# Performance work log

Measured on AMD Instinct MI355X. Metric: run time of the kernel, lower is better.

## Reference

```python
import jax, jax.numpy as jnp
import numpy as np


def _ln(x, g, b, eps=1e-5):
    mu = jnp.mean(x, axis=-1, keepdims=True)
    var = jnp.mean((x - mu) ** 2, axis=-1, keepdims=True)
    return (x - mu) * jax.lax.rsqrt(var + eps) * g + b


def setup_inputs() -> dict:
    key = jax.random.key(0)
    ks = jax.random.split(key, 12)
    B, H, W, D = 16, 128, 128, 64
    N = H * W
    Dff = 4 * D
    s = 0.02
    f32 = jnp.float32
    return {
        "x": jax.random.normal(ks[0], (B, N, D), f32),
        "H": H,
        "W": W,
        "ln1_scale": jnp.ones((D,), f32),
        "ln1_bias": jnp.zeros((D,), f32),
        "Wk": jax.random.normal(ks[1], (D, D), f32) * s,
        "bk": jnp.zeros((D,), f32),
        "Wq": jax.random.normal(ks[2], (D, D), f32) * s,
        "bq": jnp.zeros((D,), f32),
        "Wv": jax.random.normal(ks[3], (D, D), f32) * s,
        "bv": jnp.zeros((D,), f32),
        "Wr": jax.random.normal(ks[4], (D, D), f32) * s,
        "br": jnp.zeros((D,), f32),
        "ln2_scale": jnp.ones((D,), f32),
        "ln2_bias": jnp.zeros((D,), f32),
        "W1": jax.random.normal(ks[5], (Dff, D), f32) * s,
        "b1": jnp.zeros((Dff,), f32),
        "dw_w": jax.random.normal(ks[6], (Dff, 1, 3, 3), f32) * s,
        "dw_b": jnp.zeros((Dff,), f32),
        "W2": jax.random.normal(ks[7], (D, Dff), f32) * s,
        "b2": jnp.zeros((D,), f32),
    }


def reference(x, H, W, ln1_scale, ln1_bias, Wk, bk, Wq, bq, Wv, bv, Wr, br,
              ln2_scale, ln2_bias, W1, b1, dw_w, dw_b, W2, b2):
    B, N, D = x.shape
    Dff = W1.shape[0]

    # ---- EfficientAttention (head_count=1), tokens kept as [B, N, C] ----
    n1 = _ln(x, ln1_scale, ln1_bias)
    # 1x1 convs on [B,D,H,W] == per-token linear projections
    k = jax.nn.softmax(n1 @ Wk.T + bk, axis=1)    # softmax over spatial dim N (torch dim=2 of [B,Ck,N])
    q = jax.nn.softmax(n1 @ Wq.T + bq, axis=-1)   # softmax over key channels (torch dim=1)
    v = n1 @ Wv.T + bv                            # [B,N,Cv]
    context = jnp.einsum('bnk,bnv->bkv', k, v)    # key @ value^T, tiny [B,Ck,Cv]
    att = jnp.einsum('bkv,bnk->bnv', context, q)  # context^T @ query -> [B,N,Cv]
    attn_out = att @ Wr.T + br                    # reprojection 1x1 conv
    tx = x + attn_out

    # ---- MixFFN: fc1 -> depthwise 3x3 -> GELU -> fc2 ----
    n2 = _ln(tx, ln2_scale, ln2_bias)
    h = n2 @ W1.T + b1                            # [B,N,Dff]
    himg = jnp.transpose(h, (0, 2, 1)).reshape(B, Dff, H, W)
    conv = jax.lax.conv_general_dilated(
        himg, dw_w, window_strides=(1, 1), padding='SAME',
        feature_group_count=Dff,
        dimension_numbers=('NCHW', 'OIHW', 'NCHW')) + dw_b[None, :, None, None]
    h2 = jnp.transpose(conv.reshape(B, Dff, N), (0, 2, 1))
    h2 = jax.nn.gelu(h2, approximate=False)       # torch nn.GELU default is exact erf
    out = tx + (h2 @ W2.T + b2)
    return out
```

## Files before the change

kernel.cpp:

```cpp
#include <hip/hip_runtime.h>
#include <math.h>

typedef __bf16 bf16x8 __attribute__((ext_vector_type(8)));
typedef float f32x4 __attribute__((ext_vector_type(4)));
typedef float f32x2 __attribute__((ext_vector_type(2)));
typedef unsigned short u16x8 __attribute__((ext_vector_type(8)));
typedef unsigned short u16x4v __attribute__((ext_vector_type(4)));

constexpr int NIMG = 16384;
constexpr int HPITCH = 130;

__device__ __forceinline__ unsigned short f2bf(float f){
  unsigned u = __builtin_bit_cast(unsigned, f);
  u += 0x7fffu + ((u>>16)&1u);
  return (unsigned short)(u>>16);
}
__device__ __forceinline__ unsigned pack2(float a, float b){
  return (unsigned)f2bf(a) | ((unsigned)f2bf(b)<<16);
}
__device__ __forceinline__ float bf2f(unsigned short h){
  unsigned u = ((unsigned)h)<<16;
  return __builtin_bit_cast(float, u);
}
__device__ __forceinline__ bf16x8 ldfrag_g(const unsigned short* p){
  u16x8 v = *reinterpret_cast<const u16x8*>(p);
  return __builtin_bit_cast(bf16x8, v);
}
__device__ __forceinline__ f32x4 mfma16(bf16x8 a, bf16x8 b, f32x4 c){
  return __builtin_amdgcn_mfma_f32_16x16x32_bf16(a, b, c, 0, 0, 0);
}


__global__ __launch_bounds__(64) void k0_wfrag(
  const float* __restrict__ Wk, const float* __restrict__ Wq,
  const float* __restrict__ Wv, const float* __restrict__ Wr,
  const float* __restrict__ W1, const float* __restrict__ W2,
  const float* __restrict__ dww, const float* __restrict__ dwb,
  float* __restrict__ dwp, unsigned short* __restrict__ wf)
{
  const int bid = blockIdx.x, l = threadIdx.x;
  if (bid == 96){
    #pragma unroll
    for (int h=0; h<2; ++h){
      int cp = l + h*64;
      #pragma unroll
      for (int b=0; b<2; ++b){
        int slot = 2*cp + b;
        int f = ((slot&15)<<4) | (slot>>4);
        #pragma unroll
        for (int j=0;j<9;++j) dwp[cp*24 + j*2 + b] = dww[f*9+j];
        dwp[cp*24 + 18 + b] = dwb[f];
        dwp[cp*24 + 20 + b] = 0.f;
        dwp[cp*24 + 22 + b] = 0.f;
      }
    }
    return;
  }
  const float* src; int K, nt, ks; unsigned short* dst; bool perm = false;
  if (bid < 32){
    int w = bid>>3, f = bid&7;
    src = (w==0)?Wk:(w==1)?Wq:(w==2)?Wv:Wr;
    K = 64; nt = f>>1; ks = f&1;
    dst = wf + w*4096 + f*512;
  } else if (bid < 64){
    int f = bid-32; src = W1; K = 64; nt = f>>1; ks = f&1;
    dst = wf + 16384 + f*512;
  } else {
    int f = bid-64; src = W2; K = 256; nt = f>>3; ks = f&7;
    dst = wf + 32768 + f*512; perm = true;
  }
  u16x8 v;
  #pragma unroll
  for (int j=0;j<8;++j){
    int k = ks*32 + (l>>4)*8 + j;
    if (perm) k = ((k&15)<<4) | (k>>4);
    int n = nt*16 + (l&15);
    v[j] = f2bf(src[n*K + k]);
  }
  *reinterpret_cast<u16x8*>(dst + l*8) = v;
}

__global__ __launch_bounds__(256) void zhalo(unsigned* __restrict__ gh, unsigned* __restrict__ zr){
  int idx = blockIdx.x*256 + threadIdx.x;
  if (idx < 262144){
    int ch = idx & 63;
    int pos = idx >> 6;
    int side = pos & 1, row = pos >> 1;
    gh[(size_t)(row*HPITCH + side*(HPITCH-1))*64 + ch] = 0;
  } else {
    int j = idx - 262144;
    if (j < 8320) zr[j] = 0;
  }
}

__global__ __launch_bounds__(256,2) void k1_ctx(
  const float* __restrict__ x, const float* __restrict__ g1, const float* __restrict__ be1,
  const float* __restrict__ bk, const float* __restrict__ bv,
  const unsigned short* __restrict__ wf,
  float* __restrict__ g_part, float* __restrict__ g_sump)
{
  __shared__ unsigned short tiles[4][4096];
  float* ctx_l  = reinterpret_cast<float*>(&tiles[0][0]);
  float* ssum_l = ctx_l + 64*68;
  const int t = threadIdx.x, wid = t>>6, l = t&63;
  const int lg = l>>4, l15 = l&15;
  unsigned short* tile = tiles[wid];
  const int tok0 = blockIdx.x*256 + wid*64;

  bf16x8 WkF[8], WvF[8];
  #pragma unroll
  for (int f=0; f<8; ++f){
    WkF[f] = ldfrag_g(wf +    0 + f*512 + l*8);
    WvF[f] = ldfrag_g(wf + 8192 + f*512 + l*8);
  }
  float4 g1v  = *reinterpret_cast<const float4*>(&g1[l15*4]);
  float4 be1v = *reinterpret_cast<const float4*>(&be1[l15*4]);
  float bkv[4], bvv[4];
  #pragma unroll
  for (int ct=0; ct<4; ++ct){ bkv[ct]=bk[ct*16+l15]; bvv[ct]=bv[ct*16+l15]; }

  f32x4 acc[4][4];
  #pragma unroll
  for (int a=0;a<4;++a)
    #pragma unroll
    for (int b=0;b<4;++b) acc[a][b] = (f32x4){0.f,0.f,0.f,0.f};
  float sume[4] = {0.f,0.f,0.f,0.f};

  #pragma unroll
  for (int it=0; it<16; ++it){
    int row = it*4 + lg;
    float4 xv = *reinterpret_cast<const float4*>(&x[(size_t)(tok0+row)*64 + l15*4]);
    float s1 = xv.x+xv.y+xv.z+xv.w;
    float s2 = xv.x*xv.x + xv.y*xv.y + xv.z*xv.z + xv.w*xv.w;
    #pragma unroll
    for (int off=1; off<16; off<<=1){ s1 += __shfl_xor(s1,off,64); s2 += __shfl_xor(s2,off,64); }
    float mu = s1*(1.f/64.f);
    float rs = rsqrtf(s2*(1.f/64.f) - mu*mu + 1e-5f);
    uint2 pk = { pack2((xv.x-mu)*rs*g1v.x + be1v.x, (xv.y-mu)*rs*g1v.y + be1v.y),
                 pack2((xv.z-mu)*rs*g1v.z + be1v.z, (xv.w-mu)*rs*g1v.w + be1v.w) };
    *reinterpret_cast<uint2*>(&tile[row*64 + ((l15*4) ^ ((row&7)<<3))]) = pk;
  }
  bf16x8 aF[4][2];
  #pragma unroll
  for (int mt=0;mt<4;++mt){
    int row = mt*16+l15, sw=(row&7)<<3, ab=row*64;
    aF[mt][0] = __builtin_bit_cast(bf16x8, *reinterpret_cast<const u16x8*>(tile+ab+((     lg*8)^sw)));
    aF[mt][1] = __builtin_bit_cast(bf16x8, *reinterpret_cast<const u16x8*>(tile+ab+((32 + lg*8)^sw)));
  }
  #pragma unroll
  for (int half=0; half<2; ++half){
    #pragma unroll
    for (int m2=0;m2<2;++m2){
      const int mt = half*2+m2;
      #pragma unroll
      for (int ct=0;ct<4;++ct){
        f32x4 z = {0.f,0.f,0.f,0.f};
        z = mfma16(aF[mt][0], WkF[ct*2+0], z);
        z = mfma16(aF[mt][1], WkF[ct*2+1], z);
        float e0=__expf(z[0]+bkv[ct]), e1=__expf(z[1]+bkv[ct]);
        float e2=__expf(z[2]+bkv[ct]), e3=__expf(z[3]+bkv[ct]);
        sume[ct] += (e0+e1)+(e2+e3);
        const int c = ct*16+l15, sw = (c&7)<<3;
        const int cb = m2*16+lg*4;
        uint2 pe = { pack2(e0,e1), pack2(e2,e3) };
        *reinterpret_cast<uint2*>(&tile[c*64 + (cb ^ sw)]) = pe;
        f32x4 w = {0.f,0.f,0.f,0.f};
        w = mfma16(aF[mt][0], WvF[ct*2+0], w);
        w = mfma16(aF[mt][1], WvF[ct*2+1], w);
        uint2 pv = { pack2(w[0]+bvv[ct], w[1]+bvv[ct]), pack2(w[2]+bvv[ct], w[3]+bvv[ct]) };
        *reinterpret_cast<uint2*>(&tile[c*64 + ((32+cb) ^ sw)]) = pv;
      }
    }
    bf16x8 eA[4], vB[4];
    #pragma unroll
    for (int cm=0;cm<4;++cm){
      int row = cm*16+l15, sw=(row&7)<<3;
      eA[cm] = __builtin_bit_cast(bf16x8, *reinterpret_cast<const u16x8*>(tile + row*64 + ((     lg*8)^sw)));
      vB[cm] = __builtin_bit_cast(bf16x8, *reinterpret_cast<const u16x8*>(tile + row*64 + ((32 + lg*8)^sw)));
    }
    #pragma unroll
    for (int cm=0; cm<4; ++cm)
      #pragma unroll
      for (int jn=0; jn<4; ++jn)
        acc[cm][jn] = mfma16(eA[cm], vB[jn], acc[cm][jn]);
  }

  __syncthreads();
  #pragma unroll
  for (int ct=0; ct<4; ++ct){
    float s = sume[ct];
    s += __shfl_xor(s,16,64); s += __shfl_xor(s,32,64);
    if (lg==0) ssum_l[wid*64 + ct*16+l15] = s;
  }
  #define CTX_RED(OP) \
    _Pragma("unroll") for (int cm=0;cm<4;++cm) \
    _Pragma("unroll") for (int jn=0;jn<4;++jn) \
    _Pragma("unroll") for (int r=0;r<4;++r) \
      ctx_l[(cm*16+lg*4+r)*68 + jn*16+l15] OP acc[cm][jn][r];
  if (wid==0){ CTX_RED(=) }  __syncthreads();
  if (wid==1){ CTX_RED(+=) } __syncthreads();
  if (wid==2){ CTX_RED(+=) } __syncthreads();
  if (wid==3){ CTX_RED(+=) } __syncthreads();
  #undef CTX_RED
  for (int i=t; i<4096; i+=256)
    g_part[(size_t)blockIdx.x*4096 + i] = ctx_l[(i>>6)*68 + (i&63)];
  if (t<64)
    g_sump[blockIdx.x*64 + t] = ssum_l[t] + ssum_l[64+t] + ssum_l[128+t] + ssum_l[192+t];
}

__global__ __launch_bounds__(512) void k15_ctxwr(
  const float* __restrict__ g_part, const float* __restrict__ g_sump,
  const float* __restrict__ Wr, unsigned short* __restrict__ ctxWrF)
{
  __shared__ float sctx[4096];
  __shared__ float sWr[4096];
  __shared__ float sinv[64];
  const int b = blockIdx.x, t = threadIdx.x;
  if (t<64){
    float s=0.f;
    #pragma unroll 8
    for (int p=0;p<64;++p) s += g_sump[(b*64+p)*64 + t];
    sinv[t] = 1.f/s;
  }
  for (int idx=t; idx<4096; idx+=512){
    float s=0.f;
    #pragma unroll 8
    for (int p=0;p<64;++p) s += g_part[(size_t)(b*64+p)*4096 + idx];
    sctx[idx] = s;
  }
  __syncthreads();
  {
    int c = t>>3, d0 = (t&7)*8;
    float invc = sinv[c];
    #pragma unroll
    for (int dd=0; dd<8; ++dd){
      int d = d0+dd; float s = 0.f;
      #pragma unroll
      for (int v=0; v<64; ++v) s += sctx[c*64+v]*Wr[d*64+v];
      sWr[c*64+d] = s*invc;
    }
  }
  __syncthreads();
  {
    int f = t>>6, l = t&63, nt = f>>1, ks = f&1;
    u16x8 v;
    #pragma unroll
    for (int j=0;j<8;++j){
      int k = ks*32 + (l>>4)*8 + j;
      int n = nt*16 + (l&15);
      v[j] = f2bf(sWr[k*64+n]);
    }
    *reinterpret_cast<u16x8*>(ctxWrF + b*4096 + f*512 + l*8) = v;
  }
}

__global__ __launch_bounds__(256,2) void k2_attn_ffn1(
  const float* __restrict__ x,
  const float* __restrict__ g1, const float* __restrict__ be1,
  const float* __restrict__ bq, const float* __restrict__ br,
  const float* __restrict__ g2, const float* __restrict__ be2,
  const float* __restrict__ b1,
  const unsigned short* __restrict__ wf,
  const unsigned short* __restrict__ ctxWrF,
  unsigned short* __restrict__ g_txb, unsigned char* __restrict__ g_h)
{
  __shared__ unsigned short tiles[4][4096];
  const int t = threadIdx.x, wid = t>>6, l = t&63;
  const int l15 = l&15, lg = l>>4;
  unsigned short* tile = tiles[wid];
  const int tok0 = (blockIdx.x*4 + wid)*64;
  const int img  = blockIdx.x>>6;
  const int yrow = (tok0>>7)&127;
  const int xb   = tok0&127;
  const size_t hbase = ((size_t)(img*128 + yrow)*HPITCH + 1 + xb)*256;

  bf16x8 WqF[8], CWF[8];
  #pragma unroll
  for (int f=0; f<8; ++f){
    WqF[f] = ldfrag_g(wf + 4096 + f*512 + l*8);
    CWF[f] = ldfrag_g(ctxWrF + img*4096 + f*512 + l*8);
  }
  float4 g1v  = *reinterpret_cast<const float4*>(&g1[l15*4]);
  float4 be1v = *reinterpret_cast<const float4*>(&be1[l15*4]);
  float bqv[4], brv[4], g2v[4], be2v[4];
  #pragma unroll
  for (int nt=0; nt<4; ++nt){
    bqv[nt]=bq[nt*16+l15]; brv[nt]=br[nt*16+l15];
    g2v[nt]=g2[nt*16+l15]; be2v[nt]=be2[nt*16+l15];
  }
  float b1v[16];
  #pragma unroll
  for (int i=0;i<16;++i) b1v[i]=b1[i*16+l15];

  #pragma unroll
  for (int it=0; it<16; ++it){
    int row = it*4 + lg;
    float4 xv = *reinterpret_cast<const float4*>(&x[(size_t)(tok0+row)*64 + l15*4]);
    float s1 = xv.x+xv.y+xv.z+xv.w;
    float s2 = xv.x*xv.x + xv.y*xv.y + xv.z*xv.z + xv.w*xv.w;
    #pragma unroll
    for (int off=1; off<16; off<<=1){ s1 += __shfl_xor(s1,off,64); s2 += __shfl_xor(s2,off,64); }
    float mu = s1*(1.f/64.f);
    float rs = rsqrtf(s2*(1.f/64.f) - mu*mu + 1e-5f);
    uint2 pk = { pack2((xv.x-mu)*rs*g1v.x + be1v.x, (xv.y-mu)*rs*g1v.y + be1v.y),
                 pack2((xv.z-mu)*rs*g1v.z + be1v.z, (xv.w-mu)*rs*g1v.w + be1v.w) };
    *reinterpret_cast<uint2*>(&tile[row*64 + ((l15*4) ^ ((row&7)<<3))]) = pk;
  }

  for (int mt=0; mt<4; ++mt){
    const int arow = mt*16 + l15;
    const int asw  = (arow&7)<<3;
    const int abase= arow*64;
    bf16x8 a0 = __builtin_bit_cast(bf16x8, *reinterpret_cast<const u16x8*>(tile + abase + ((     lg*8) ^ asw)));
    bf16x8 a1 = __builtin_bit_cast(bf16x8, *reinterpret_cast<const u16x8*>(tile + abase + ((32 + lg*8) ^ asw)));
    f32x4 qa[4];
    #pragma unroll
    for (int nt=0; nt<4; ++nt){
      f32x4 z = {0.f,0.f,0.f,0.f};
      z = mfma16(a0, WqF[nt*2+0], z);
      z = mfma16(a1, WqF[nt*2+1], z);
      qa[nt] = z;
    }
    #pragma unroll
    for (int nt=0; nt<4; ++nt)
      #pragma unroll
      for (int r=0; r<4; ++r) qa[nt][r] += bqv[nt];
    float mx[4];
    #pragma unroll
    for (int r=0;r<4;++r) mx[r] = fmaxf(fmaxf(qa[0][r],qa[1][r]), fmaxf(qa[2][r],qa[3][r]));
    #pragma unroll
    for (int off=1; off<16; off<<=1)
      #pragma unroll
      for (int r=0;r<4;++r) mx[r] = fmaxf(mx[r], __shfl_xor(mx[r], off, 64));
    float sm[4] = {0.f,0.f,0.f,0.f};
    #pragma unroll
    for (int nt=0;nt<4;++nt)
      #pragma unroll
      for (int r=0;r<4;++r){ float e = __expf(qa[nt][r]-mx[r]); qa[nt][r]=e; sm[r]+=e; }
    #pragma unroll
    for (int off=1; off<16; off<<=1)
      #pragma unroll
      for (int r=0;r<4;++r) sm[r] += __shfl_xor(sm[r], off, 64);
    float inv[4];
    #pragma unroll
    for (int r=0;r<4;++r) inv[r] = 1.f/sm[r];
    #pragma unroll
    for (int nt=0;nt<4;++nt)
      #pragma unroll
      for (int r=0;r<4;++r){
        int row = mt*16 + lg*4 + r, col = nt*16 + l15;
        tile[row*64 + (col ^ ((row&7)<<3))] = f2bf(qa[nt][r]*inv[r]);
      }
    bf16x8 p0 = __builtin_bit_cast(bf16x8, *reinterpret_cast<const u16x8*>(tile + abase + ((     lg*8) ^ asw)));
    bf16x8 p1 = __builtin_bit_cast(bf16x8, *reinterpret_cast<const u16x8*>(tile + abase + ((32 + lg*8) ^ asw)));
    f32x4 ao[4];
    #pragma unroll
    for (int nt=0; nt<4; ++nt){
      f32x4 z = {0.f,0.f,0.f,0.f};
      z = mfma16(p0, CWF[nt*2+0], z);
      z = mfma16(p1, CWF[nt*2+1], z);
      ao[nt] = z;
    }
    float txv[4][4];
    float s1v[4] = {0.f,0.f,0.f,0.f}, s2v[4] = {0.f,0.f,0.f,0.f};
    #pragma unroll
    for (int nt=0;nt<4;++nt)
      #pragma unroll
      for (int r=0;r<4;++r){
        size_t row = (size_t)(tok0 + mt*16 + lg*4 + r);
        float v = ao[nt][r] + brv[nt] + x[row*64 + nt*16+l15];
        g_txb[row*64 + nt*16+l15] = f2bf(v);
        txv[nt][r] = v; s1v[r] += v; s2v[r] += v*v;
      }
    #pragma unroll
    for (int off=1; off<16; off<<=1)
      #pragma unroll
      for (int r=0;r<4;++r){ s1v[r] += __shfl_xor(s1v[r], off, 64); s2v[r] += __shfl_xor(s2v[r], off, 64); }
    #pragma unroll
    for (int r=0;r<4;++r){
      float mu2 = s1v[r]*(1.f/64.f);
      float rs  = rsqrtf(s2v[r]*(1.f/64.f) - mu2*mu2 + 1e-5f);
      s1v[r] = mu2; s2v[r] = rs;
    }
    #pragma unroll
    for (int nt=0;nt<4;++nt)
      #pragma unroll
      for (int r=0;r<4;++r){
        int row = mt*16 + lg*4 + r, col = nt*16 + l15;
        float n2 = (txv[nt][r]-s1v[r])*s2v[r]*g2v[nt] + be2v[nt];
        tile[row*64 + (col ^ ((row&7)<<3))] = f2bf(n2);
      }
  }

  for (int mt=0; mt<4; ++mt){
    const int arow = mt*16 + l15;
    const int asw  = (arow&7)<<3;
    const int abase= arow*64;
    bf16x8 n20 = __builtin_bit_cast(bf16x8, *reinterpret_cast<const u16x8*>(tile + abase + ((     lg*8) ^ asw)));
    bf16x8 n21 = __builtin_bit_cast(bf16x8, *reinterpret_cast<const u16x8*>(tile + abase + ((32 + lg*8) ^ asw)));
    unsigned hq[4][4];
    #pragma unroll
    for (int np=0; np<8; ++np){
      bf16x8 wa0 = ldfrag_g(wf + 16384 + (np*4+0)*512 + l*8);
      bf16x8 wa1 = ldfrag_g(wf + 16384 + (np*4+1)*512 + l*8);
      bf16x8 wb0 = ldfrag_g(wf + 16384 + (np*4+2)*512 + l*8);
      bf16x8 wb1 = ldfrag_g(wf + 16384 + (np*4+3)*512 + l*8);
      float ba = b1v[np*2], bb = b1v[np*2+1];
      f32x4 ha = {ba,ba,ba,ba};
      ha = mfma16(n20, wa0, ha);
      ha = mfma16(n21, wa1, ha);
      f32x4 hb = {bb,bb,bb,bb};
      hb = mfma16(n20, wb0, hb);
      hb = mfma16(n21, wb1, hb);
      const int d = np>>1;
      if ((np&1)==0){
        #pragma unroll
        for (int r=0;r<4;++r)
          hq[r][d] = (unsigned)__builtin_amdgcn_cvt_pk_fp8_f32(ha[r], hb[r], 0, false);
      } else {
        #pragma unroll
        for (int r=0;r<4;++r)
          hq[r][d] = (unsigned)__builtin_amdgcn_cvt_pk_fp8_f32(ha[r], hb[r], (int)hq[r][d], true);
      }
    }
    #pragma unroll
    for (int r=0;r<4;++r){
      const size_t ro = hbase + (size_t)(mt*16+lg*4+r)*256 + l15*16;
      uint4 v = { hq[r][0], hq[r][1], hq[r][2], hq[r][3] };
      *reinterpret_cast<uint4*>(g_h + ro) = v;
    }
  }
}

__global__ __launch_bounds__(256,4) void k3_conv_ffn2(
  const unsigned char* __restrict__ g_h,
  const unsigned char* __restrict__ zrow,
  const float* __restrict__ dwp,
  const float* __restrict__ b2,
  const unsigned short* __restrict__ wf,
  const unsigned short* __restrict__ g_txb, float* __restrict__ out)
{
  __shared__ unsigned ring[4][1170];
  __shared__ unsigned short obuf[2][4096];
  const int t = threadIdx.x, w = t>>6, l = t&63;
  const int l15 = l&15, lg = l>>4;
  const int bid = (blockIdx.x & 7)*128 + (blockIdx.x >> 3);
  const int img = bid>>6;
  const int r6  = bid&63;
  const int y0  = (r6>>3)*16, x0 = (r6&7)*16;

  const int cp = t & 127;
  const int pg = t >> 7;
  f32x2 tp[9];
  #pragma unroll
  for (int j=0;j<9;++j)
    tp[j] = *reinterpret_cast<const f32x2*>(&dwp[cp*24 + j*2]);
  const f32x2 cb2 = *reinterpret_cast<const f32x2*>(&dwp[cp*24 + 18]);

  bf16x8 W2F[8];
  #pragma unroll
  for (int q=0;q<8;++q)
    W2F[q] = ldfrag_g(wf + 32768 + (w*8 + q)*512 + l*8);
  const float4 b2q = *reinterpret_cast<const float4*>(&b2[w*16 + lg*4]);

  const int pi = 1 + (t>>4);
  const int c0 = (t&15)*16;

  auto rowsrc = [&](int ri) -> const unsigned char* {
    return (ri>=0 && ri<128)
      ? g_h + ((size_t)(img*128+ri)*HPITCH + x0)*256
      : zrow + x0*256;
  };
  auto ldrow = [&](int ri, uint4* m, unsigned* h){
    const unsigned char* src = rowsrc(ri);
    *m = *reinterpret_cast<const uint4*>(src + pi*256 + c0);
    if (t < 128){
      int ph = (t<64)?0:17, dh = t&63;
      *h = reinterpret_cast<const unsigned*>(src + ph*256)[dh];
    }
  };
  auto wrrow = [&](int sl, uint4 m, unsigned h){
    unsigned* rg = ring[sl];
    const int base = pi*65 + (c0>>2);
    rg[base+0] = m.x; rg[base+1] = m.y; rg[base+2] = m.z; rg[base+3] = m.w;
    if (t < 128){
      int ph = (t<64)?0:17, dh = t&63;
      rg[ph*65 + dh] = h;
    }
  };

  {
    uint4 m0,m1,m2; unsigned h0=0,h1=0,h2=0;
    ldrow(y0-1,&m0,&h0); ldrow(y0,&m1,&h1); ldrow(y0+1,&m2,&h2);
    wrrow(0,m0,h0); wrrow(1,m1,h1); wrrow(2,m2,h2);
  }
  __syncthreads();

  const f32x2 kC0 = {-2.3022082f,-2.3022082f};
  const f32x2 kC1 = {-0.1029432f,-0.1029432f};

  for (int yy=0; yy<16; ++yy){
    const int gy = y0 + yy;
    uint4 rm; unsigned rh = 0;
    ldrow(gy+2, &rm, &rh);
    const size_t gtok = (size_t)img*16384 + (size_t)gy*128 + x0 + l15;
    const u16x4v tq = *reinterpret_cast<const u16x4v*>(&g_txb[gtok*64 + w*16 + lg*4]);

    {
      const unsigned short* rA = reinterpret_cast<const unsigned short*>(ring[(yy  )&3]);
      const unsigned short* rB = reinterpret_cast<const unsigned short*>(ring[(yy+1)&3]);
      const unsigned short* rC = reinterpret_cast<const unsigned short*>(ring[(yy+2)&3]);
      unsigned short* ob = obuf[yy&1];
      const int rb = pg*8;
      f32x2 PA = __builtin_amdgcn_cvt_pk_f32_fp8((int)rA[(rb  )*130 + cp], false);
      f32x2 PB = __builtin_amdgcn_cvt_pk_f32_fp8((int)rB[(rb  )*130 + cp], false);
      f32x2 PC = __builtin_amdgcn_cvt_pk_f32_fp8((int)rC[(rb  )*130 + cp], false);
      f32x2 CA = __builtin_amdgcn_cvt_pk_f32_fp8((int)rA[(rb+1)*130 + cp], false);
      f32x2 CB = __builtin_amdgcn_cvt_pk_f32_fp8((int)rB[(rb+1)*130 + cp], false);
      f32x2 CC = __builtin_amdgcn_cvt_pk_f32_fp8((int)rC[(rb+1)*130 + cp], false);
      #pragma unroll
      for (int i=0;i<8;++i){
        const int ro = (rb+i+2)*130 + cp;
        f32x2 NA = __builtin_amdgcn_cvt_pk_f32_fp8((int)rA[ro], false);
        f32x2 NB = __builtin_amdgcn_cvt_pk_f32_fp8((int)rB[ro], false);
        f32x2 NC = __builtin_amdgcn_cvt_pk_f32_fp8((int)rC[ro], false);
        f32x2 a = cb2;
        a += tp[0]*PA; a += tp[1]*CA; a += tp[2]*NA;
        a += tp[3]*PB; a += tp[4]*CB; a += tp[5]*NB;
        a += tp[6]*PC; a += tp[7]*CC; a += tp[8]*NC;
        f32x2 u = a*a;
        f32x2 wv = u*kC1 + kC0;
        f32x2 arg = a*wv;
        f32x2 e;
        e[0]=__builtin_amdgcn_exp2f(arg[0]); e[1]=__builtin_amdgcn_exp2f(arg[1]);
        f32x2 den = e + (f32x2){1.f,1.f};
        f32x2 rc;
        rc[0]=__builtin_amdgcn_rcpf(den[0]); rc[1]=__builtin_amdgcn_rcpf(den[1]);
        f32x2 g = a*rc;
        unsigned pk;
        asm("v_cvt_pk_bf16_f32 %0, %1, %2" : "=v"(pk) : "v"(g[0]), "v"(g[1]));
        const int p = rb + i;
        *reinterpret_cast<unsigned*>(&ob[p*256 + ((2*cp) ^ ((p&7)<<3))]) = pk;
        PA=CA; PB=CB; PC=CC; CA=NA; CB=NB; CC=NC;
      }
    }

    wrrow((yy+3)&3, rm, rh);
    __syncthreads();

    f32x4 oacc = {0.f,0.f,0.f,0.f};
    const int nsw = (l15&7)<<3;
    const unsigned short* ob = obuf[yy&1];
    #pragma unroll
    for (int i=0;i<4;++i){
      bf16x8 fb0 = __builtin_bit_cast(bf16x8,
        *reinterpret_cast<const u16x8*>(&ob[l15*256 + ((i*64      + lg*8) ^ nsw)]));
      bf16x8 fb1 = __builtin_bit_cast(bf16x8,
        *reinterpret_cast<const u16x8*>(&ob[l15*256 + ((i*64 + 32 + lg*8) ^ nsw)]));
      oacc = mfma16(W2F[i*2+0], fb0, oacc);
      oacc = mfma16(W2F[i*2+1], fb1, oacc);
    }
    float4 o;
    o.x = oacc[0] + b2q.x + bf2f(tq[0]);
    o.y = oacc[1] + b2q.y + bf2f(tq[1]);
    o.z = oacc[2] + b2q.z + bf2f(tq[2]);
    o.w = oacc[3] + b2q.w + bf2f(tq[3]);
    *reinterpret_cast<float4*>(&out[gtok*64 + w*16 + lg*4]) = o;
  }
}

extern "C" void kernel_launch(void* const* d_in, const int* in_sizes, int n_in,
                              void* d_out, int out_size, void* d_ws, size_t ws_size,
                              hipStream_t stream)
{
  const float* x  =(const float*)d_in[0];
  const float* g1 =(const float*)d_in[3];
  const float* be1=(const float*)d_in[4];
  const float* Wk =(const float*)d_in[5];
  const float* bk =(const float*)d_in[6];
  const float* Wq =(const float*)d_in[7];
  const float* bq =(const float*)d_in[8];
  const float* Wv =(const float*)d_in[9];
  const float* bv =(const float*)d_in[10];
  const float* Wr =(const float*)d_in[11];
  const float* br =(const float*)d_in[12];
  const float* g2 =(const float*)d_in[13];
  const float* be2=(const float*)d_in[14];
  const float* W1 =(const float*)d_in[15];
  const float* b1 =(const float*)d_in[16];
  const float* dww=(const float*)d_in[17];
  const float* dwb=(const float*)d_in[18];
  const float* W2 =(const float*)d_in[19];
  const float* b2 =(const float*)d_in[20];
  float* outp = (float*)d_out;
  char* ws = (char*)d_ws;

  unsigned short* wfb    = (unsigned short*)ws;
  unsigned short* ctxWrF = (unsigned short*)(ws + 98304);
  float* g_sump = (float*)(ws + 229376);
  float* g_part = (float*)(ws + 524288);
  unsigned short* g_txb = (unsigned short*)(ws + 17825792);
  unsigned char* g_h    = (unsigned char*)(ws + 51380224);
  unsigned char* zr     = (unsigned char*)(ws + 119537664);
  float* dwp            = (float*)(ws + 119603200);

  hipLaunchKernelGGL(k0_wfrag, dim3(97), dim3(64), 0, stream, Wk, Wq, Wv, Wr, W1, W2, dww, dwb, dwp, wfb);
  hipLaunchKernelGGL(zhalo, dim3(1057), dim3(256), 0, stream, (unsigned*)g_h, (unsigned*)zr);
  hipLaunchKernelGGL(k1_ctx, dim3(1024), dim3(256), 0, stream, x, g1, be1, bk, bv, wfb, g_part, g_sump);
  hipLaunchKernelGGL(k15_ctxwr, dim3(16), dim3(512), 0, stream, g_part, g_sump, Wr, ctxWrF);
  hipLaunchKernelGGL(k2_attn_ffn1, dim3(1024), dim3(256), 0, stream,
                     x, g1, be1, bq, br, g2, be2, b1, wfb, ctxWrF, g_txb, g_h);
  hipLaunchKernelGGL(k3_conv_ffn2, dim3(1024), dim3(256), 0, stream,
                     g_h, zr, dwp, b2, wfb, g_txb, outp);
}
```

Measured before the change: 203.3 us.

## Compute query softmax in k1 and pass it to k2 through global memory

Moves the query projection and its softmax from k2 into k1, which already holds the LayerNorm-1 tile. The result is written to a new bf16 global buffer, so k2 no longer recomputes LN1 or Q; it loads the softmaxed query fragments directly. This removes the duplicated LayerNorm and Q matmul work from k2. In exchange it adds a 32 MB write in k1 and a matching read in k2, and k1 gains extra work and register pressure.

New measurement: 203.5 us. Within noise of the previous version (+0.1%).

```diff
diff --git a/kernel.cpp b/kernel.cpp
--- a/kernel.cpp
+++ b/kernel.cpp
@@ -95,9 +95,10 @@
 
 __global__ __launch_bounds__(256,2) void k1_ctx(
   const float* __restrict__ x, const float* __restrict__ g1, const float* __restrict__ be1,
-  const float* __restrict__ bk, const float* __restrict__ bv,
+  const float* __restrict__ bk, const float* __restrict__ bq, const float* __restrict__ bv,
   const unsigned short* __restrict__ wf,
-  float* __restrict__ g_part, float* __restrict__ g_sump)
+  float* __restrict__ g_part, float* __restrict__ g_sump,
+  unsigned short* __restrict__ qs)
 {
   __shared__ unsigned short tiles[4][4096];
   float* ctx_l  = reinterpret_cast<float*>(&tiles[0][0]);
@@ -107,24 +108,8 @@
   unsigned short* tile = tiles[wid];
   const int tok0 = blockIdx.x*256 + wid*64;
 
-  bf16x8 WkF[8], WvF[8];
-  #pragma unroll
-  for (int f=0; f<8; ++f){
-    WkF[f] = ldfrag_g(wf +    0 + f*512 + l*8);
-    WvF[f] = ldfrag_g(wf + 8192 + f*512 + l*8);
-  }
   float4 g1v  = *reinterpret_cast<const float4*>(&g1[l15*4]);
   float4 be1v = *reinterpret_cast<const float4*>(&be1[l15*4]);
-  float bkv[4], bvv[4];
-  #pragma unroll
-  for (int ct=0; ct<4; ++ct){ bkv[ct]=bk[ct*16+l15]; bvv[ct]=bv[ct*16+l15]; }
-
-  f32x4 acc[4][4];
-  #pragma unroll
-  for (int a=0;a<4;++a)
-    #pragma unroll
-    for (int b=0;b<4;++b) acc[a][b] = (f32x4){0.f,0.f,0.f,0.f};
-  float sume[4] = {0.f,0.f,0.f,0.f};
 
   #pragma unroll
   for (int it=0; it<16; ++it){
@@ -147,6 +132,78 @@
     aF[mt][0] = __builtin_bit_cast(bf16x8, *reinterpret_cast<const u16x8*>(tile+ab+((     lg*8)^sw)));
     aF[mt][1] = __builtin_bit_cast(bf16x8, *reinterpret_cast<const u16x8*>(tile+ab+((32 + lg*8)^sw)));
   }
+
+  {
+    float bqv[4];
+    #pragma unroll
+    for (int ct=0; ct<4; ++ct) bqv[ct]=bq[ct*16+l15];
+    #pragma unroll
+    for (int mt=0; mt<4; ++mt){
+      f32x4 qa[4];
+      #pragma unroll
+      for (int nt=0; nt<4; ++nt){
+        bf16x8 w0 = ldfrag_g(wf + 4096 + (nt*2+0)*512 + l*8);
+        bf16x8 w1 = ldfrag_g(wf + 4096 + (nt*2+1)*512 + l*8);
+        f32x4 z = {0.f,0.f,0.f,0.f};
+        z = mfma16(aF[mt][0], w0, z);
+        z = mfma16(aF[mt][1], w1, z);
+        #pragma unroll
+        for (int r=0;r<4;++r) z[r] += bqv[nt];
+        qa[nt] = z;
+      }
+      float mx[4];
+      #pragma unroll
+      for (int r=0;r<4;++r) mx[r] = fmaxf(fmaxf(qa[0][r],qa[1][r]), fmaxf(qa[2][r],qa[3][r]));
+      #pragma unroll
+      for (int off=1; off<16; off<<=1)
+        #pragma unroll
+        for (int r=0;r<4;++r) mx[r] = fmaxf(mx[r], __shfl_xor(mx[r], off, 64));
+      float sm[4] = {0.f,0.f,0.f,0.f};
+      #pragma unroll
+      for (int nt=0;nt<4;++nt)
+        #pragma unroll
+        for (int r=0;r<4;++r){ float e = __expf(qa[nt][r]-mx[r]); qa[nt][r]=e; sm[r]+=e; }
+      #pragma unroll
+      for (int off=1; off<16; off<<=1)
+        #pragma unroll
+        for (int r=0;r<4;++r) sm[r] += __shfl_xor(sm[r], off, 64);
+      float inv[4];
+      #pragma unroll
+      for (int r=0;r<4;++r) inv[r] = 1.f/sm[r];
+      #pragma unroll
+      for (int nt=0;nt<4;++nt)
+        #pragma unroll
+        for (int r=0;r<4;++r){
+          int row = mt*16 + lg*4 + r, col = nt*16 + l15;
+          tile[row*64 + (col ^ ((row&7)<<3))] = f2bf(qa[nt][r]*inv[r]);
+        }
+    }
+    #pragma unroll
+    for (int c=0;c<8;++c){
+      int idx = c*64 + l;
+      int tok = idx>>3, b8 = (idx&7)*8;
+      u16x8 v = *reinterpret_cast<const u16x8*>(tile + tok*64 + (b8 ^ ((tok&7)<<3)));
+      *reinterpret_cast<u16x8*>(qs + (size_t)(tok0+tok)*64 + b8) = v;
+    }
+  }
+
+  bf16x8 WkF[8], WvF[8];
+  #pragma unroll
+  for (int f=0; f<8; ++f){
+    WkF[f] = ldfrag_g(wf +    0 + f*512 + l*8);
+    WvF[f] = ldfrag_g(wf + 8192 + f*512 + l*8);
+  }
+  float bkv[4], bvv[4];
+  #pragma unroll
+  for (int ct=0; ct<4; ++ct){ bkv[ct]=bk[ct*16+l15]; bvv[ct]=bv[ct*16+l15]; }
+
+  f32x4 acc[4][4];
+  #pragma unroll
+  for (int a=0;a<4;++a)
+    #pragma unroll
+    for (int b=0;b<4;++b) acc[a][b] = (f32x4){0.f,0.f,0.f,0.f};
+  float sume[4] = {0.f,0.f,0.f,0.f};
+
   #pragma unroll
   for (int half=0; half<2; ++half){
     #pragma unroll
@@ -256,12 +313,12 @@
 
 __global__ __launch_bounds__(256,2) void k2_attn_ffn1(
   const float* __restrict__ x,
-  const float* __restrict__ g1, const float* __restrict__ be1,
-  const float* __restrict__ bq, const float* __restrict__ br,
+  const float* __restrict__ br,
   const float* __restrict__ g2, const float* __restrict__ be2,
   const float* __restrict__ b1,
   const unsigned short* __restrict__ wf,
   const unsigned short* __restrict__ ctxWrF,
+  const unsigned short* __restrict__ qs,
   unsigned short* __restrict__ g_txb, unsigned char* __restrict__ g_h)
 {
   __shared__ unsigned short tiles[4][4096];
@@ -274,85 +331,24 @@
   const int xb   = tok0&127;
   const size_t hbase = ((size_t)(img*128 + yrow)*HPITCH + 1 + xb)*256;
 
-  bf16x8 WqF[8], CWF[8];
-  #pragma unroll
-  for (int f=0; f<8; ++f){
-    WqF[f] = ldfrag_g(wf + 4096 + f*512 + l*8);
+  bf16x8 CWF[8];
+  #pragma unroll
+  for (int f=0; f<8; ++f)
     CWF[f] = ldfrag_g(ctxWrF + img*4096 + f*512 + l*8);
-  }
-  float4 g1v  = *reinterpret_cast<const float4*>(&g1[l15*4]);
-  float4 be1v = *reinterpret_cast<const float4*>(&be1[l15*4]);
-  float bqv[4], brv[4], g2v[4], be2v[4];
+  float brv[4], g2v[4], be2v[4];
   #pragma unroll
   for (int nt=0; nt<4; ++nt){
-    bqv[nt]=bq[nt*16+l15]; brv[nt]=br[nt*16+l15];
+    brv[nt]=br[nt*16+l15];
     g2v[nt]=g2[nt*16+l15]; be2v[nt]=be2[nt*16+l15];
   }
   float b1v[16];
   #pragma unroll
   for (int i=0;i<16;++i) b1v[i]=b1[i*16+l15];
 
-  #pragma unroll
-  for (int it=0; it<16; ++it){
-    int row = it*4 + lg;
-    float4 xv = *reinterpret_cast<const float4*>(&x[(size_t)(tok0+row)*64 + l15*4]);
-    float s1 = xv.x+xv.y+xv.z+xv.w;
-    float s2 = xv.x*xv.x + xv.y*xv.y + xv.z*xv.z + xv.w*xv.w;
-    #pragma unroll
-    for (int off=1; off<16; off<<=1){ s1 += __shfl_xor(s1,off,64); s2 += __shfl_xor(s2,off,64); }
-    float mu = s1*(1.f/64.f);
-    float rs = rsqrtf(s2*(1.f/64.f) - mu*mu + 1e-5f);
-    uint2 pk = { pack2((xv.x-mu)*rs*g1v.x + be1v.x, (xv.y-mu)*rs*g1v.y + be1v.y),
-                 pack2((xv.z-mu)*rs*g1v.z + be1v.z, (xv.w-mu)*rs*g1v.w + be1v.w) };
-    *reinterpret_cast<uint2*>(&tile[row*64 + ((l15*4) ^ ((row&7)<<3))]) = pk;
-  }
-
   for (int mt=0; mt<4; ++mt){
-    const int arow = mt*16 + l15;
-    const int asw  = (arow&7)<<3;
-    const int abase= arow*64;
-    bf16x8 a0 = __builtin_bit_cast(bf16x8, *reinterpret_cast<const u16x8*>(tile + abase + ((     lg*8) ^ asw)));
-    bf16x8 a1 = __builtin_bit_cast(bf16x8, *reinterpret_cast<const u16x8*>(tile + abase + ((32 + lg*8) ^ asw)));
-    f32x4 qa[4];
-    #pragma unroll
-    for (int nt=0; nt<4; ++nt){
-      f32x4 z = {0.f,0.f,0.f,0.f};
-      z = mfma16(a0, WqF[nt*2+0], z);
-      z = mfma16(a1, WqF[nt*2+1], z);
-      qa[nt] = z;
-    }
-    #pragma unroll
-    for (int nt=0; nt<4; ++nt)
-      #pragma unroll
-      for (int r=0; r<4; ++r) qa[nt][r] += bqv[nt];
-    float mx[4];
-    #pragma unroll
-    for (int r=0;r<4;++r) mx[r] = fmaxf(fmaxf(qa[0][r],qa[1][r]), fmaxf(qa[2][r],qa[3][r]));
-    #pragma unroll
-    for (int off=1; off<16; off<<=1)
-      #pragma unroll
-      for (int r=0;r<4;++r) mx[r] = fmaxf(mx[r], __shfl_xor(mx[r], off, 64));
-    float sm[4] = {0.f,0.f,0.f,0.f};
-    #pragma unroll
-    for (int nt=0;nt<4;++nt)
-      #pragma unroll
-      for (int r=0;r<4;++r){ float e = __expf(qa[nt][r]-mx[r]); qa[nt][r]=e; sm[r]+=e; }
-    #pragma unroll
-    for (int off=1; off<16; off<<=1)
-      #pragma unroll
-      for (int r=0;r<4;++r) sm[r] += __shfl_xor(sm[r], off, 64);
-    float inv[4];
-    #pragma unroll
-    for (int r=0;r<4;++r) inv[r] = 1.f/sm[r];
-    #pragma unroll
-    for (int nt=0;nt<4;++nt)
-      #pragma unroll
-      for (int r=0;r<4;++r){
-        int row = mt*16 + lg*4 + r, col = nt*16 + l15;
-        tile[row*64 + (col ^ ((row&7)<<3))] = f2bf(qa[nt][r]*inv[r]);
-      }
-    bf16x8 p0 = __builtin_bit_cast(bf16x8, *reinterpret_cast<const u16x8*>(tile + abase + ((     lg*8) ^ asw)));
-    bf16x8 p1 = __builtin_bit_cast(bf16x8, *reinterpret_cast<const u16x8*>(tile + abase + ((32 + lg*8) ^ asw)));
+    const size_t qrow = (size_t)(tok0 + mt*16 + l15)*64;
+    bf16x8 p0 = ldfrag_g(qs + qrow + lg*8);
+    bf16x8 p1 = ldfrag_g(qs + qrow + 32 + lg*8);
     f32x4 ao[4];
     #pragma unroll
     for (int nt=0; nt<4; ++nt){
@@ -603,13 +599,14 @@
   unsigned char* g_h    = (unsigned char*)(ws + 51380224);
   unsigned char* zr     = (unsigned char*)(ws + 119537664);
   float* dwp            = (float*)(ws + 119603200);
+  unsigned short* qsb   = (unsigned short*)(ws + 119668736);
 
   hipLaunchKernelGGL(k0_wfrag, dim3(97), dim3(64), 0, stream, Wk, Wq, Wv, Wr, W1, W2, dww, dwb, dwp, wfb);
   hipLaunchKernelGGL(zhalo, dim3(1057), dim3(256), 0, stream, (unsigned*)g_h, (unsigned*)zr);
-  hipLaunchKernelGGL(k1_ctx, dim3(1024), dim3(256), 0, stream, x, g1, be1, bk, bv, wfb, g_part, g_sump);
+  hipLaunchKernelGGL(k1_ctx, dim3(1024), dim3(256), 0, stream, x, g1, be1, bk, bq, bv, wfb, g_part, g_sump, qsb);
   hipLaunchKernelGGL(k15_ctxwr, dim3(16), dim3(512), 0, stream, g_part, g_sump, Wr, ctxWrF);
   hipLaunchKernelGGL(k2_attn_ffn1, dim3(1024), dim3(256), 0, stream,
-                     x, g1, be1, bq, br, g2, be2, b1, wfb, ctxWrF, g_txb, g_h);
+                     x, br, g2, be2, b1, wfb, ctxWrF, qsb, g_txb, g_h);
   hipLaunchKernelGGL(k3_conv_ffn2, dim3(1024), dim3(256), 0, stream,
                      g_h, zr, dwp, b2, wfb, g_txb, outp);
 }
```
